# Kernel optimization log

Hardware: AMD Instinct MI355X
Metric: run time of the kernel (lower is better)

Reference implementation:

```python
import jax, jax.numpy as jnp
import numpy as np

N_NODES = 50000
N_EDGES = 800000
N_FEATS = 64
K_HOPS = 3


def setup_inputs() -> dict:
    key = jax.random.key(0)
    k1, k2, k3 = jax.random.split(key, 3)
    x = jax.random.normal(k1, (N_NODES, N_FEATS), dtype=jnp.float32)
    edge_index = jax.random.randint(k2, (2, N_EDGES), 0, N_NODES, dtype=jnp.int32)
    # SGConv linear: out_channels = 1 (hardcoded in Net)
    W = jax.random.normal(k3, (1, N_FEATS), dtype=jnp.float32) / np.sqrt(N_FEATS)
    b = jnp.zeros((1,), dtype=jnp.float32)
    return {"x": x, "edge_index": edge_index, "W": W, "b": b}


def reference(x, edge_index, W, b):
    # SGConv: X' = (D^-1/2 (A + I) D^-1/2)^K X @ W.T + b
    N = x.shape[0]
    self_loops = jnp.arange(N, dtype=edge_index.dtype)
    row = jnp.concatenate([edge_index[0], self_loops])  # source nodes (x_j)
    col = jnp.concatenate([edge_index[1], self_loops])  # destination nodes
    # gcn_norm: degree computed at destination with unit edge weights
    deg = jax.ops.segment_sum(jnp.ones(row.shape[0], x.dtype), col, num_segments=N)
    dinv = jnp.where(deg > 0, jax.lax.rsqrt(deg), jnp.zeros_like(deg))
    norm = dinv[row] * dinv[col]  # [E + N]
    # K hops of normalized sparse propagation: out[col] += norm * x[row]
    for _ in range(K_HOPS):
        x = jax.ops.segment_sum(norm[:, None] * x[row], col, num_segments=N)
    return x @ W.T + b  # [N, 1]
```

## Files before the change

### kernel.cpp

```cpp
#include <hip/hip_runtime.h>

#define N_NODES 50000
#define N_EDGES 800000
#define N_FEATS 64
#define EB4     (N_EDGES / 4)
#define NBUCK   256
#define BRANGE  196
#define CAPB    4096
#define NTHR    1024
#define CHUNK   ((EB4 + NBUCK - 1) / NBUCK)
#define MAXREC  (CHUNK * 4)
#define MVBASE  784

struct SmemSort { unsigned buf[MAXREC]; unsigned adr[MAXREC]; };


__global__ void __launch_bounds__(NTHR) k_bucketize(
    const int* __restrict__ row, const int* __restrict__ col,
    const float* __restrict__ x, const float* __restrict__ w,
    int* __restrict__ gcur, unsigned* __restrict__ recs,
    float* __restrict__ mv)
{
    __shared__ SmemSort u;
    __shared__ int s_cnt[NBUCK];
    __shared__ int s_off[NBUCK];
    __shared__ int s_wsum[4];
    __shared__ int s_total;

    const int t = threadIdx.x;
    const int blk = blockIdx.x;

    if (t < NBUCK) s_cnt[t] = 0;
    __syncthreads();

    const int g = blk * CHUNK + t;
    const bool valid = (t < CHUNK) && (g < EB4);
    int4 c4, r4;
    int bk0, bk1, bk2, bk3, rk0, rk1, rk2, rk3;
    if (valid) {
        c4 = ((const int4*)col)[g];
        r4 = ((const int4*)row)[g];
        bk0 = c4.x / BRANGE; rk0 = atomicAdd(&s_cnt[bk0], 1);
        bk1 = c4.y / BRANGE; rk1 = atomicAdd(&s_cnt[bk1], 1);
        bk2 = c4.z / BRANGE; rk2 = atomicAdd(&s_cnt[bk2], 1);
        bk3 = c4.w / BRANGE; rk3 = atomicAdd(&s_cnt[bk3], 1);
    }

    {
        const int un = t - MVBASE;
        const int node = blk * BRANGE + un;
        if (un >= 0 && un < BRANGE && node < N_NODES) {
            const float4* xr = (const float4*)(x + (size_t)node * N_FEATS);
            const float4* wr = (const float4*)w;
            float a = 0.0f;
            #pragma unroll
            for (int k = 0; k < N_FEATS / 4; k++) {
                const float4 v = xr[k];
                const float4 q = wr[k];
                a += v.x * q.x + v.y * q.y + v.z * q.z + v.w * q.w;
            }
            mv[node] = a;
        }
    }
    __syncthreads();

    if (t < NBUCK) {
        const int lane = t & 63;
        const int cnt = s_cnt[t];
        int val = cnt;
        #pragma unroll
        for (int d = 1; d < 64; d <<= 1) {
            int tmp = __shfl_up(val, d);
            if (lane >= d) val += tmp;
        }
        if (lane == 63) s_wsum[t >> 6] = val;
        s_off[t] = val - cnt;
    }
    __syncthreads();
    if (t < NBUCK) {
        const int w4 = t >> 6;
        int base = 0;
        #pragma unroll
        for (int i = 0; i < 3; i++) if (i < w4) base += s_wsum[i];
        s_off[t] += base;
        const int cnt = s_cnt[t];
        s_cnt[t] = cnt ? atomicAdd(&gcur[t], cnt) : 0;
        if (t == 0) s_total = s_wsum[0] + s_wsum[1] + s_wsum[2] + s_wsum[3];
    }
    __syncthreads();

    if (valid) {
        const int cc[4] = {c4.x, c4.y, c4.z, c4.w};
        const int rr[4] = {r4.x, r4.y, r4.z, r4.w};
        const int bb[4] = {bk0, bk1, bk2, bk3};
        const int kk[4] = {rk0, rk1, rk2, rk3};
        #pragma unroll
        for (int i = 0; i < 4; i++) {
            const int b = bb[i];
            const int p = s_off[b] + kk[i];
            const int slot = s_cnt[b] + kk[i];
            u.buf[p] = ((unsigned)(cc[i] - b * BRANGE) << 16) | (unsigned)rr[i];
            u.adr[p] = (slot < CAPB) ? (unsigned)(b * CAPB + slot) : 0xFFFFFFFFu;
        }
    }
    __syncthreads();

    const int total = s_total;
    for (int p = t; p < total; p += NTHR) {
        const unsigned a = u.adr[p];
        if (a != 0xFFFFFFFFu) recs[a] = u.buf[p];
    }
}

__global__ void __launch_bounds__(NTHR) k_prep(
    const int* __restrict__ gcur, const unsigned* __restrict__ recs,
    const float* __restrict__ mv, float* __restrict__ dinv,
    float* __restrict__ z0)
{
    __shared__ int s_deg[BRANGE];
    const int t = threadIdx.x;
    const int blk = blockIdx.x;
    if (t < BRANGE) s_deg[t] = 0;
    __syncthreads();

    const int sz = min(gcur[blk], CAPB);
    const int szw = (sz + 3) >> 2;
    const uint4* rb4 = (const uint4*)(recs + (size_t)blk * CAPB);
    if (t < szw) {
        const uint4 r = rb4[t];
        const int b4 = t << 2;
        if (b4 + 0 < sz) atomicAdd(&s_deg[r.x >> 16], 1);
        if (b4 + 1 < sz) atomicAdd(&s_deg[r.y >> 16], 1);
        if (b4 + 2 < sz) atomicAdd(&s_deg[r.z >> 16], 1);
        if (b4 + 3 < sz) atomicAdd(&s_deg[r.w >> 16], 1);
    }
    __syncthreads();

    if (t < BRANGE) {
        const int node = blk * BRANGE + t;
        if (node < N_NODES) {
            const float d = rsqrtf((float)(s_deg[t] + 1));
            dinv[node] = d;
            z0[node] = d * mv[node];
        }
    }
}

template <bool FINAL>
__global__ void __launch_bounds__(NTHR) k_hop(
    const int* __restrict__ gcur, const unsigned* __restrict__ recs,
    const float* __restrict__ dinv, const float* __restrict__ zin,
    float* __restrict__ out, const float* __restrict__ bptr)
{
    __shared__ float s_acc[BRANGE];
    const int t = threadIdx.x;
    const int blk = blockIdx.x;
    if (t < BRANGE) s_acc[t] = 0.0f;
    __syncthreads();

    const int sz  = min(gcur[blk], CAPB);
    const int sz4 = sz >> 2;
    const uint4* rb4 = (const uint4*)(recs + (size_t)blk * CAPB);
    for (int e = t; e < sz4; e += NTHR) {
        const uint4 r = rb4[e];
        const float v0 = zin[r.x & 0xFFFFu];
        const float v1 = zin[r.y & 0xFFFFu];
        const float v2 = zin[r.z & 0xFFFFu];
        const float v3 = zin[r.w & 0xFFFFu];
        atomicAdd(&s_acc[r.x >> 16], v0);
        atomicAdd(&s_acc[r.y >> 16], v1);
        atomicAdd(&s_acc[r.z >> 16], v2);
        atomicAdd(&s_acc[r.w >> 16], v3);
    }
    if (t < (sz & 3)) {
        const unsigned r = recs[(size_t)blk * CAPB + (sz4 << 2) + t];
        atomicAdd(&s_acc[r >> 16], zin[r & 0xFFFFu]);
    }
    __syncthreads();

    if (t < BRANGE) {
        const int node = blk * BRANGE + t;
        if (node < N_NODES) {
            const float d = dinv[node];
            const float v = zin[node] + s_acc[t];
            out[node] = FINAL ? (d * v + bptr[0]) : (d * d * v);
        }
    }
}


extern "C" void kernel_launch(void* const* d_in, const int* in_sizes, int n_in,
                              void* d_out, int out_size, void* d_ws, size_t ws_size,
                              hipStream_t stream) {
    const float* x  = (const float*)d_in[0];
    const int*   ei = (const int*)d_in[1];
    const float* W  = (const float*)d_in[2];
    const float* b  = (const float*)d_in[3];
    float* out = (float*)d_out;

    const int* row = ei;
    const int* col = ei + N_EDGES;

    int*      gcur = (int*)d_ws;
    unsigned* recs = (unsigned*)(gcur + NBUCK);
    float*    mv   = (float*)(recs + (size_t)NBUCK * CAPB);
    float*    dinv = mv + N_NODES;
    float*    z0   = dinv + N_NODES;
    float*    z1   = z0 + N_NODES;

    hipMemsetAsync(gcur, 0, NBUCK * sizeof(int), stream);

    k_bucketize<<<dim3(NBUCK), dim3(NTHR), 0, stream>>>(row, col, x, W, gcur, recs, mv);
    k_prep<<<dim3(NBUCK), dim3(NTHR), 0, stream>>>(gcur, recs, mv, dinv, z0);
    k_hop<false><<<dim3(NBUCK), dim3(NTHR), 0, stream>>>(gcur, recs, dinv, z0, z1, nullptr);
    k_hop<false><<<dim3(NBUCK), dim3(NTHR), 0, stream>>>(gcur, recs, dinv, z1, z0, nullptr);
    k_hop<true ><<<dim3(NBUCK), dim3(NTHR), 0, stream>>>(gcur, recs, dinv, z0, out, b);
}
```

Before: 101.5 us.

## Fuse prep and three hops into one persistent kernel with grid barriers

Replaces the prep kernel and three hop launches with one persistent kernel of 256 blocks that synchronises through software grid barriers built from per-block magic flags in workspace. Each block's edge records are loaded into LDS once and reused across all hops, and dinv and z are kept in shared memory. Source indices are remapped to a padded per-bucket stride so each block's z values land in its own region. This removes launch gaps and repeated record reads, but relies on all 256 blocks being co-resident for the spin barrier, and the stale magic values from a previous run could let a barrier pass early unless bars is reset.

After: 107.8 us. +6.2%, slower.

```diff
diff --git a/kernel.cpp b/kernel.cpp
--- a/kernel.cpp
+++ b/kernel.cpp
@@ -6,14 +6,61 @@
 #define EB4     (N_EDGES / 4)
 #define NBUCK   256
 #define BRANGE  196
+#define ZSTRIDE 208
 #define CAPB    4096
 #define NTHR    1024
 #define CHUNK   ((EB4 + NBUCK - 1) / NBUCK)
 #define MAXREC  (CHUNK * 4)
 #define MVBASE  784
+#define MAGICK(k) (0x9E3779B9u + ((unsigned)(k) << 8))
 
 struct SmemSort { unsigned buf[MAXREC]; unsigned adr[MAXREC]; };
 
+__device__ __forceinline__ void st_agent(float* p, float v) {
+    __hip_atomic_store(p, v, __ATOMIC_RELAXED, __HIP_MEMORY_SCOPE_AGENT);
+}
+__device__ __forceinline__ void st_agent_u(unsigned* p, unsigned v) {
+    __hip_atomic_store(p, v, __ATOMIC_RELAXED, __HIP_MEMORY_SCOPE_AGENT);
+}
+__device__ __forceinline__ unsigned ld_agent_u(const unsigned* p) {
+    return __hip_atomic_load(p, __ATOMIC_RELAXED, __HIP_MEMORY_SCOPE_AGENT);
+}
+
+__device__ __forceinline__ void gbar(unsigned* bars, int k) {
+    const unsigned magic = MAGICK(k);
+    unsigned* slots = bars + k * NBUCK;
+    __syncthreads();
+    if (threadIdx.x == 0) st_agent_u(&slots[blockIdx.x], magic);
+    int n;
+    do {
+        __builtin_amdgcn_s_sleep(2);
+        unsigned v = (threadIdx.x < NBUCK) ? ld_agent_u(&slots[threadIdx.x]) : magic;
+        n = __syncthreads_count(v == magic);
+    } while (n < NTHR);
+}
+
+__device__ __forceinline__ void gather(const unsigned* recs_l, int sz,
+                                       const float* __restrict__ zin,
+                                       float* s_acc) {
+    const int t = threadIdx.x;
+    const int sz4 = sz >> 2;
+    const uint4* rl4 = (const uint4*)recs_l;
+    for (int e = t; e < sz4; e += NTHR) {
+        const uint4 r = rl4[e];
+        const float v0 = zin[r.x & 0xFFFFu];
+        const float v1 = zin[r.y & 0xFFFFu];
+        const float v2 = zin[r.z & 0xFFFFu];
+        const float v3 = zin[r.w & 0xFFFFu];
+        atomicAdd(&s_acc[r.x >> 16], v0);
+        atomicAdd(&s_acc[r.y >> 16], v1);
+        atomicAdd(&s_acc[r.z >> 16], v2);
+        atomicAdd(&s_acc[r.w >> 16], v3);
+    }
+    if (t < (sz & 3)) {
+        const unsigned r = recs_l[(sz4 << 2) + t];
+        atomicAdd(&s_acc[r >> 16], zin[r & 0xFFFFu]);
+    }
+}
 
 __global__ void __launch_bounds__(NTHR) k_bucketize(
     const int* __restrict__ row, const int* __restrict__ col,
@@ -99,7 +146,9 @@
             const int b = bb[i];
             const int p = s_off[b] + kk[i];
             const int slot = s_cnt[b] + kk[i];
-            u.buf[p] = ((unsigned)(cc[i] - b * BRANGE) << 16) | (unsigned)rr[i];
+            const unsigned src = (unsigned)rr[i];
+            const unsigned psrc = src + 12u * (src / (unsigned)BRANGE);
+            u.buf[p] = ((unsigned)(cc[i] - b * BRANGE) << 16) | psrc;
             u.adr[p] = (slot < CAPB) ? (unsigned)(b * CAPB + slot) : 0xFFFFFFFFu;
         }
     }
@@ -112,80 +161,86 @@
     }
 }
 
-__global__ void __launch_bounds__(NTHR) k_prep(
+__global__ void __launch_bounds__(NTHR) k_main(
     const int* __restrict__ gcur, const unsigned* __restrict__ recs,
-    const float* __restrict__ mv, float* __restrict__ dinv,
-    float* __restrict__ z0)
+    const float* __restrict__ mv, const float* __restrict__ bptr,
+    float* __restrict__ out, unsigned* __restrict__ bars,
+    float* __restrict__ zA, float* __restrict__ zB, float* __restrict__ zC)
 {
-    __shared__ int s_deg[BRANGE];
+    __shared__ unsigned recs_l[CAPB];
+    __shared__ int      s_deg[BRANGE];
+    __shared__ float    s_dinv[BRANGE];
+    __shared__ float    s_z[BRANGE];
+    __shared__ float    s_acc[BRANGE];
+
     const int t = threadIdx.x;
     const int blk = blockIdx.x;
+    const int node = blk * BRANGE + t;
+
+    const int sz  = min(gcur[blk], CAPB);
+    const int szw = (sz + 3) >> 2;
+
     if (t < BRANGE) s_deg[t] = 0;
-    __syncthreads();
-
-    const int sz = min(gcur[blk], CAPB);
-    const int szw = (sz + 3) >> 2;
+
+    uint4 rv = make_uint4(0u, 0u, 0u, 0u);
     const uint4* rb4 = (const uint4*)(recs + (size_t)blk * CAPB);
+    if (t < szw) rv = rb4[t];
+    float mvv = 0.0f;
+    if (t < BRANGE && node < N_NODES) mvv = mv[node];
+    __syncthreads();
+
     if (t < szw) {
-        const uint4 r = rb4[t];
+        ((uint4*)recs_l)[t] = rv;
         const int b4 = t << 2;
-        if (b4 + 0 < sz) atomicAdd(&s_deg[r.x >> 16], 1);
-        if (b4 + 1 < sz) atomicAdd(&s_deg[r.y >> 16], 1);
-        if (b4 + 2 < sz) atomicAdd(&s_deg[r.z >> 16], 1);
-        if (b4 + 3 < sz) atomicAdd(&s_deg[r.w >> 16], 1);
+        if (b4 + 0 < sz) atomicAdd(&s_deg[rv.x >> 16], 1);
+        if (b4 + 1 < sz) atomicAdd(&s_deg[rv.y >> 16], 1);
+        if (b4 + 2 < sz) atomicAdd(&s_deg[rv.z >> 16], 1);
+        if (b4 + 3 < sz) atomicAdd(&s_deg[rv.w >> 16], 1);
     }
     __syncthreads();
 
     if (t < BRANGE) {
-        const int node = blk * BRANGE + t;
+        const float d = rsqrtf((float)(s_deg[t] + 1));
+        s_dinv[t] = d;
+        s_acc[t] = 0.0f;
         if (node < N_NODES) {
-            const float d = rsqrtf((float)(s_deg[t] + 1));
-            dinv[node] = d;
-            z0[node] = d * mv[node];
-        }
-    }
-}
-
-template <bool FINAL>
-__global__ void __launch_bounds__(NTHR) k_hop(
-    const int* __restrict__ gcur, const unsigned* __restrict__ recs,
-    const float* __restrict__ dinv, const float* __restrict__ zin,
-    float* __restrict__ out, const float* __restrict__ bptr)
-{
-    __shared__ float s_acc[BRANGE];
-    const int t = threadIdx.x;
-    const int blk = blockIdx.x;
-    if (t < BRANGE) s_acc[t] = 0.0f;
-    __syncthreads();
-
-    const int sz  = min(gcur[blk], CAPB);
-    const int sz4 = sz >> 2;
-    const uint4* rb4 = (const uint4*)(recs + (size_t)blk * CAPB);
-    for (int e = t; e < sz4; e += NTHR) {
-        const uint4 r = rb4[e];
-        const float v0 = zin[r.x & 0xFFFFu];
-        const float v1 = zin[r.y & 0xFFFFu];
-        const float v2 = zin[r.z & 0xFFFFu];
-        const float v3 = zin[r.w & 0xFFFFu];
-        atomicAdd(&s_acc[r.x >> 16], v0);
-        atomicAdd(&s_acc[r.y >> 16], v1);
-        atomicAdd(&s_acc[r.z >> 16], v2);
-        atomicAdd(&s_acc[r.w >> 16], v3);
-    }
-    if (t < (sz & 3)) {
-        const unsigned r = recs[(size_t)blk * CAPB + (sz4 << 2) + t];
-        atomicAdd(&s_acc[r >> 16], zin[r & 0xFFFFu]);
-    }
-    __syncthreads();
-
+            const float zv = d * mvv;
+            s_z[t] = zv;
+            st_agent(&zA[blk * ZSTRIDE + t], zv);
+        }
+    }
+    gbar(bars, 0);
+
+    gather(recs_l, sz, zA, s_acc);
+    __syncthreads();
     if (t < BRANGE) {
-        const int node = blk * BRANGE + t;
         if (node < N_NODES) {
-            const float d = dinv[node];
-            const float v = zin[node] + s_acc[t];
-            out[node] = FINAL ? (d * v + bptr[0]) : (d * d * v);
-        }
-    }
+            const float d = s_dinv[t];
+            const float nz = d * d * (s_z[t] + s_acc[t]);
+            s_z[t] = nz;
+            st_agent(&zB[blk * ZSTRIDE + t], nz);
+        }
+        s_acc[t] = 0.0f;
+    }
+    gbar(bars, 1);
+
+    gather(recs_l, sz, zB, s_acc);
+    __syncthreads();
+    if (t < BRANGE) {
+        if (node < N_NODES) {
+            const float d = s_dinv[t];
+            const float nz = d * d * (s_z[t] + s_acc[t]);
+            s_z[t] = nz;
+            st_agent(&zC[blk * ZSTRIDE + t], nz);
+        }
+        s_acc[t] = 0.0f;
+    }
+    gbar(bars, 2);
+
+    gather(recs_l, sz, zC, s_acc);
+    __syncthreads();
+    if (t < BRANGE && node < N_NODES)
+        out[node] = s_dinv[t] * (s_z[t] + s_acc[t]) + bptr[0];
 }
 
 
@@ -201,18 +256,16 @@
     const int* row = ei;
     const int* col = ei + N_EDGES;
 
-    int*      gcur = (int*)d_ws;
+    unsigned* bars = (unsigned*)d_ws;
+    int*      gcur = (int*)(bars + 3 * NBUCK);
     unsigned* recs = (unsigned*)(gcur + NBUCK);
     float*    mv   = (float*)(recs + (size_t)NBUCK * CAPB);
-    float*    dinv = mv + N_NODES;
-    float*    z0   = dinv + N_NODES;
-    float*    z1   = z0 + N_NODES;
+    float*    zA   = mv + N_NODES;
+    float*    zB   = zA + (size_t)NBUCK * ZSTRIDE;
+    float*    zC   = zB + (size_t)NBUCK * ZSTRIDE;
 
     hipMemsetAsync(gcur, 0, NBUCK * sizeof(int), stream);
 
     k_bucketize<<<dim3(NBUCK), dim3(NTHR), 0, stream>>>(row, col, x, W, gcur, recs, mv);
-    k_prep<<<dim3(NBUCK), dim3(NTHR), 0, stream>>>(gcur, recs, mv, dinv, z0);
-    k_hop<false><<<dim3(NBUCK), dim3(NTHR), 0, stream>>>(gcur, recs, dinv, z0, z1, nullptr);
-    k_hop<false><<<dim3(NBUCK), dim3(NTHR), 0, stream>>>(gcur, recs, dinv, z1, z0, nullptr);
-    k_hop<true ><<<dim3(NBUCK), dim3(NTHR), 0, stream>>>(gcur, recs, dinv, z0, out, b);
-}
+    k_main<<<dim3(NBUCK), dim3(NTHR), 0, stream>>>(gcur, recs, mv, b, out, bars, zA, zB, zC);
+}
```

## Sort bucket records by destination and combine same-destination atomics in hops

Applied to the files above, without the earlier changes.

k_prep now counting-sorts each bucket's edge records by destination node in shared memory and writes them back. k_hop can then sum consecutive records with equal destinations in registers before issuing a shared-memory atomic. The x·W matvec moves from bucketize into k_prep, and bucketize uses a fully occupied grid sized to the edge count. The extra sort pass in k_prep is traded for fewer LDS atomic conflicts across three hops.

Result: faster. 96.71 us (-4.7%).

```diff
diff --git a/kernel.cpp b/kernel.cpp
--- a/kernel.cpp
+++ b/kernel.cpp
@@ -7,19 +7,17 @@
 #define NBUCK   256
 #define BRANGE  196
 #define CAPB    4096
-#define NTHR    1024
-#define CHUNK   ((EB4 + NBUCK - 1) / NBUCK)
-#define MAXREC  (CHUNK * 4)
-#define MVBASE  784
+#define BZT     1024
+#define PRT     512
+#define HOPT    1024
+#define MAXREC  (BZT * 4)
 
 struct SmemSort { unsigned buf[MAXREC]; unsigned adr[MAXREC]; };
 
 
-__global__ void __launch_bounds__(NTHR) k_bucketize(
+__global__ void __launch_bounds__(BZT) k_bucketize(
     const int* __restrict__ row, const int* __restrict__ col,
-    const float* __restrict__ x, const float* __restrict__ w,
-    int* __restrict__ gcur, unsigned* __restrict__ recs,
-    float* __restrict__ mv)
+    int* __restrict__ gcur, unsigned* __restrict__ recs)
 {
     __shared__ SmemSort u;
     __shared__ int s_cnt[NBUCK];
@@ -28,126 +26,160 @@
     __shared__ int s_total;
 
     const int t = threadIdx.x;
-    const int blk = blockIdx.x;
-
     if (t < NBUCK) s_cnt[t] = 0;
     __syncthreads();
 
-    const int g = blk * CHUNK + t;
-    const bool valid = (t < CHUNK) && (g < EB4);
+    const int g = blockIdx.x * BZT + t;
+    const bool valid = g < EB4;
     int4 c4, r4;
-    int bk0, bk1, bk2, bk3, rk0, rk1, rk2, rk3;
+    int bk[4], rk[4];
     if (valid) {
         c4 = ((const int4*)col)[g];
         r4 = ((const int4*)row)[g];
-        bk0 = c4.x / BRANGE; rk0 = atomicAdd(&s_cnt[bk0], 1);
-        bk1 = c4.y / BRANGE; rk1 = atomicAdd(&s_cnt[bk1], 1);
-        bk2 = c4.z / BRANGE; rk2 = atomicAdd(&s_cnt[bk2], 1);
-        bk3 = c4.w / BRANGE; rk3 = atomicAdd(&s_cnt[bk3], 1);
-    }
-
-    {
-        const int un = t - MVBASE;
-        const int node = blk * BRANGE + un;
-        if (un >= 0 && un < BRANGE && node < N_NODES) {
+        bk[0] = c4.x / BRANGE; rk[0] = atomicAdd(&s_cnt[bk[0]], 1);
+        bk[1] = c4.y / BRANGE; rk[1] = atomicAdd(&s_cnt[bk[1]], 1);
+        bk[2] = c4.z / BRANGE; rk[2] = atomicAdd(&s_cnt[bk[2]], 1);
+        bk[3] = c4.w / BRANGE; rk[3] = atomicAdd(&s_cnt[bk[3]], 1);
+    }
+    __syncthreads();
+
+    if (t < NBUCK) {
+        const int lane = t & 63;
+        const int cnt = s_cnt[t];
+        int val = cnt;
+        #pragma unroll
+        for (int d = 1; d < 64; d <<= 1) {
+            int tmp = __shfl_up(val, d);
+            if (lane >= d) val += tmp;
+        }
+        if (lane == 63) s_wsum[t >> 6] = val;
+        s_off[t] = val - cnt;
+    }
+    __syncthreads();
+    if (t < NBUCK) {
+        const int w4 = t >> 6;
+        int base = 0;
+        #pragma unroll
+        for (int i = 0; i < 3; i++) if (i < w4) base += s_wsum[i];
+        s_off[t] += base;
+        const int cnt = s_cnt[t];
+        s_cnt[t] = cnt ? atomicAdd(&gcur[t], cnt) : 0;
+        if (t == 0) s_total = s_wsum[0] + s_wsum[1] + s_wsum[2] + s_wsum[3];
+    }
+    __syncthreads();
+
+    if (valid) {
+        const int cc[4] = {c4.x, c4.y, c4.z, c4.w};
+        const int rr[4] = {r4.x, r4.y, r4.z, r4.w};
+        #pragma unroll
+        for (int i = 0; i < 4; i++) {
+            const int b = bk[i];
+            const int p = s_off[b] + rk[i];
+            const int slot = s_cnt[b] + rk[i];
+            u.buf[p] = ((unsigned)(cc[i] - b * BRANGE) << 16) | (unsigned)rr[i];
+            u.adr[p] = (slot < CAPB) ? (unsigned)(b * CAPB + slot) : 0xFFFFFFFFu;
+        }
+    }
+    __syncthreads();
+
+    const int total = s_total;
+    for (int p = t; p < total; p += BZT) {
+        const unsigned a = u.adr[p];
+        if (a != 0xFFFFFFFFu) recs[a] = u.buf[p];
+    }
+}
+
+__global__ void __launch_bounds__(PRT) k_prep(
+    const int* __restrict__ gcur, unsigned* __restrict__ recs,
+    const float* __restrict__ x, const float* __restrict__ w,
+    float* __restrict__ dinv, float* __restrict__ z0)
+{
+    __shared__ unsigned s_sorted[CAPB];
+    __shared__ int s_deg[NBUCK];
+    __shared__ int s_base[NBUCK];
+    __shared__ int s_wsum[4];
+
+    const int t = threadIdx.x;
+    const int blk = blockIdx.x;
+    if (t < NBUCK) s_deg[t] = 0;
+    __syncthreads();
+
+    const int sz = min(gcur[blk], CAPB);
+
+    const uint2* rb2 = (const uint2*)(recs + (size_t)blk * CAPB);
+    uint2 q[4];
+    #pragma unroll
+    for (int i = 0; i < 4; i++) {
+        const int idx = t + i * PRT;
+        q[i] = make_uint2(0u, 0u);
+        if (2 * idx < sz) {
+            q[i] = rb2[idx];
+            atomicAdd(&s_deg[q[i].x >> 16], 1);
+            if (2 * idx + 1 < sz) atomicAdd(&s_deg[q[i].y >> 16], 1);
+        }
+    }
+    __syncthreads();
+
+    if (t < NBUCK) {
+        const int lane = t & 63;
+        const int c = s_deg[t];
+        int v = c;
+        #pragma unroll
+        for (int d = 1; d < 64; d <<= 1) {
+            int tmp = __shfl_up(v, d);
+            if (lane >= d) v += tmp;
+        }
+        if (lane == 63) s_wsum[t >> 6] = v;
+        s_base[t] = v - c;
+    }
+    __syncthreads();
+    if (t < NBUCK) {
+        const int w4 = t >> 6;
+        int base = 0;
+        #pragma unroll
+        for (int i = 0; i < 3; i++) if (i < w4) base += s_wsum[i];
+        s_base[t] += base;
+    }
+    __syncthreads();
+
+    #pragma unroll
+    for (int i = 0; i < 4; i++) {
+        const int idx = t + i * PRT;
+        if (2 * idx < sz) {
+            const int p0 = atomicAdd(&s_base[q[i].x >> 16], 1);
+            s_sorted[p0] = q[i].x;
+            if (2 * idx + 1 < sz) {
+                const int p1 = atomicAdd(&s_base[q[i].y >> 16], 1);
+                s_sorted[p1] = q[i].y;
+            }
+        }
+    }
+    __syncthreads();
+
+    for (int p = t; p < sz; p += PRT)
+        recs[(size_t)blk * CAPB + p] = s_sorted[p];
+
+    if (t < BRANGE) {
+        const int node = blk * BRANGE + t;
+        if (node < N_NODES) {
+            const float d = rsqrtf((float)(s_deg[t] + 1));
+            dinv[node] = d;
             const float4* xr = (const float4*)(x + (size_t)node * N_FEATS);
             const float4* wr = (const float4*)w;
             float a = 0.0f;
             #pragma unroll
             for (int k = 0; k < N_FEATS / 4; k++) {
                 const float4 v = xr[k];
-                const float4 q = wr[k];
-                a += v.x * q.x + v.y * q.y + v.z * q.z + v.w * q.w;
+                const float4 u = wr[k];
+                a += v.x * u.x + v.y * u.y + v.z * u.z + v.w * u.w;
             }
-            mv[node] = a;
-        }
-    }
-    __syncthreads();
-
-    if (t < NBUCK) {
-        const int lane = t & 63;
-        const int cnt = s_cnt[t];
-        int val = cnt;
-        #pragma unroll
-        for (int d = 1; d < 64; d <<= 1) {
-            int tmp = __shfl_up(val, d);
-            if (lane >= d) val += tmp;
-        }
-        if (lane == 63) s_wsum[t >> 6] = val;
-        s_off[t] = val - cnt;
-    }
-    __syncthreads();
-    if (t < NBUCK) {
-        const int w4 = t >> 6;
-        int base = 0;
-        #pragma unroll
-        for (int i = 0; i < 3; i++) if (i < w4) base += s_wsum[i];
-        s_off[t] += base;
-        const int cnt = s_cnt[t];
-        s_cnt[t] = cnt ? atomicAdd(&gcur[t], cnt) : 0;
-        if (t == 0) s_total = s_wsum[0] + s_wsum[1] + s_wsum[2] + s_wsum[3];
-    }
-    __syncthreads();
-
-    if (valid) {
-        const int cc[4] = {c4.x, c4.y, c4.z, c4.w};
-        const int rr[4] = {r4.x, r4.y, r4.z, r4.w};
-        const int bb[4] = {bk0, bk1, bk2, bk3};
-        const int kk[4] = {rk0, rk1, rk2, rk3};
-        #pragma unroll
-        for (int i = 0; i < 4; i++) {
-            const int b = bb[i];
-            const int p = s_off[b] + kk[i];
-            const int slot = s_cnt[b] + kk[i];
-            u.buf[p] = ((unsigned)(cc[i] - b * BRANGE) << 16) | (unsigned)rr[i];
-            u.adr[p] = (slot < CAPB) ? (unsigned)(b * CAPB + slot) : 0xFFFFFFFFu;
-        }
-    }
-    __syncthreads();
-
-    const int total = s_total;
-    for (int p = t; p < total; p += NTHR) {
-        const unsigned a = u.adr[p];
-        if (a != 0xFFFFFFFFu) recs[a] = u.buf[p];
-    }
-}
-
-__global__ void __launch_bounds__(NTHR) k_prep(
-    const int* __restrict__ gcur, const unsigned* __restrict__ recs,
-    const float* __restrict__ mv, float* __restrict__ dinv,
-    float* __restrict__ z0)
-{
-    __shared__ int s_deg[BRANGE];
-    const int t = threadIdx.x;
-    const int blk = blockIdx.x;
-    if (t < BRANGE) s_deg[t] = 0;
-    __syncthreads();
-
-    const int sz = min(gcur[blk], CAPB);
-    const int szw = (sz + 3) >> 2;
-    const uint4* rb4 = (const uint4*)(recs + (size_t)blk * CAPB);
-    if (t < szw) {
-        const uint4 r = rb4[t];
-        const int b4 = t << 2;
-        if (b4 + 0 < sz) atomicAdd(&s_deg[r.x >> 16], 1);
-        if (b4 + 1 < sz) atomicAdd(&s_deg[r.y >> 16], 1);
-        if (b4 + 2 < sz) atomicAdd(&s_deg[r.z >> 16], 1);
-        if (b4 + 3 < sz) atomicAdd(&s_deg[r.w >> 16], 1);
-    }
-    __syncthreads();
-
-    if (t < BRANGE) {
-        const int node = blk * BRANGE + t;
-        if (node < N_NODES) {
-            const float d = rsqrtf((float)(s_deg[t] + 1));
-            dinv[node] = d;
-            z0[node] = d * mv[node];
+            z0[node] = d * a;
         }
     }
 }
 
 template <bool FINAL>
-__global__ void __launch_bounds__(NTHR) k_hop(
+__global__ void __launch_bounds__(HOPT) k_hop(
     const int* __restrict__ gcur, const unsigned* __restrict__ recs,
     const float* __restrict__ dinv, const float* __restrict__ zin,
     float* __restrict__ out, const float* __restrict__ bptr)
@@ -161,16 +193,19 @@
     const int sz  = min(gcur[blk], CAPB);
     const int sz4 = sz >> 2;
     const uint4* rb4 = (const uint4*)(recs + (size_t)blk * CAPB);
-    for (int e = t; e < sz4; e += NTHR) {
+    for (int e = t; e < sz4; e += HOPT) {
         const uint4 r = rb4[e];
         const float v0 = zin[r.x & 0xFFFFu];
         const float v1 = zin[r.y & 0xFFFFu];
         const float v2 = zin[r.z & 0xFFFFu];
         const float v3 = zin[r.w & 0xFFFFu];
-        atomicAdd(&s_acc[r.x >> 16], v0);
-        atomicAdd(&s_acc[r.y >> 16], v1);
-        atomicAdd(&s_acc[r.z >> 16], v2);
-        atomicAdd(&s_acc[r.w >> 16], v3);
+        const unsigned d0 = r.x >> 16, d1 = r.y >> 16;
+        const unsigned d2 = r.z >> 16, d3 = r.w >> 16;
+        float s = v0;
+        if (d1 == d0) s += v1; else { atomicAdd(&s_acc[d0], s); s = v1; }
+        if (d2 == d1) s += v2; else { atomicAdd(&s_acc[d1], s); s = v2; }
+        if (d3 == d2) s += v3; else { atomicAdd(&s_acc[d2], s); s = v3; }
+        atomicAdd(&s_acc[d3], s);
     }
     if (t < (sz & 3)) {
         const unsigned r = recs[(size_t)blk * CAPB + (sz4 << 2) + t];
@@ -203,16 +238,15 @@
 
     int*      gcur = (int*)d_ws;
     unsigned* recs = (unsigned*)(gcur + NBUCK);
-    float*    mv   = (float*)(recs + (size_t)NBUCK * CAPB);
-    float*    dinv = mv + N_NODES;
+    float*    dinv = (float*)(recs + (size_t)NBUCK * CAPB);
     float*    z0   = dinv + N_NODES;
     float*    z1   = z0 + N_NODES;
 
     hipMemsetAsync(gcur, 0, NBUCK * sizeof(int), stream);
 
-    k_bucketize<<<dim3(NBUCK), dim3(NTHR), 0, stream>>>(row, col, x, W, gcur, recs, mv);
-    k_prep<<<dim3(NBUCK), dim3(NTHR), 0, stream>>>(gcur, recs, mv, dinv, z0);
-    k_hop<false><<<dim3(NBUCK), dim3(NTHR), 0, stream>>>(gcur, recs, dinv, z0, z1, nullptr);
-    k_hop<false><<<dim3(NBUCK), dim3(NTHR), 0, stream>>>(gcur, recs, dinv, z1, z0, nullptr);
-    k_hop<true ><<<dim3(NBUCK), dim3(NTHR), 0, stream>>>(gcur, recs, dinv, z0, out, b);
-}
+    k_bucketize<<<(EB4 + BZT - 1) / BZT, BZT, 0, stream>>>(row, col, gcur, recs);
+    k_prep<<<NBUCK, PRT, 0, stream>>>(gcur, recs, x, W, dinv, z0);
+    k_hop<false><<<NBUCK, HOPT, 0, stream>>>(gcur, recs, dinv, z0, z1, nullptr);
+    k_hop<false><<<NBUCK, HOPT, 0, stream>>>(gcur, recs, dinv, z1, z0, nullptr);
+    k_hop<true ><<<NBUCK, HOPT, 0, stream>>>(gcur, recs, dinv, z0, out, b);
+}
```
